# Performance work log

Measured on AMD Instinct MI355X. Metric: run time of the kernel, lower is better.

The kernel has to match this reference:

```python
import jax, jax.numpy as jnp
import numpy as np

N_TOKEN = 32000
D_MODEL = 1024
N_HEAD = 16
D_HEAD = 64
D_INNER = 4096
N_LAYER = 2
QLEN = 256
MLEN = 256
BSZ = 8


def setup_inputs() -> dict:
    key = jax.random.key(0)
    ks = jax.random.split(key, 16)
    s = 0.02  # init scale
    inp = {}
    inp['dec_inp'] = jax.random.randint(ks[0], (QLEN, BSZ), 0, N_TOKEN, dtype=jnp.int32)
    inp['target'] = jax.random.randint(ks[1], (QLEN, BSZ), 0, N_TOKEN, dtype=jnp.int32)
    inp['valid_mask'] = jnp.ones((QLEN, BSZ), jnp.float32)
    inp['mems'] = jax.random.normal(ks[2], (N_LAYER, MLEN, BSZ, D_MODEL), jnp.float32)
    inp['vocab_emb'] = jax.random.normal(ks[3], (N_TOKEN, D_MODEL), jnp.float32) * s
    inp['out_w'] = jax.random.normal(ks[4], (N_TOKEN, D_MODEL), jnp.float32) * s
    inp['out_b'] = jnp.zeros((N_TOKEN,), jnp.float32)
    inp['qkv_w'] = jax.random.normal(ks[5], (N_LAYER, D_MODEL, 3 * N_HEAD * D_HEAD), jnp.float32) * s
    inp['r_w'] = jax.random.normal(ks[6], (N_LAYER, D_MODEL, N_HEAD * D_HEAD), jnp.float32) * s
    inp['o_w'] = jax.random.normal(ks[7], (N_LAYER, N_HEAD * D_HEAD, D_MODEL), jnp.float32) * s
    inp['ln1_g'] = jnp.ones((N_LAYER, D_MODEL), jnp.float32)
    inp['ln1_b'] = jnp.zeros((N_LAYER, D_MODEL), jnp.float32)
    inp['ff_w1'] = jax.random.normal(ks[8], (N_LAYER, D_MODEL, D_INNER), jnp.float32) * s
    inp['ff_b1'] = jnp.zeros((N_LAYER, D_INNER), jnp.float32)
    inp['ff_w2'] = jax.random.normal(ks[9], (N_LAYER, D_INNER, D_MODEL), jnp.float32) * s
    inp['ff_b2'] = jnp.zeros((N_LAYER, D_MODEL), jnp.float32)
    inp['ln2_g'] = jnp.ones((N_LAYER, D_MODEL), jnp.float32)
    inp['ln2_b'] = jnp.zeros((N_LAYER, D_MODEL), jnp.float32)
    inp['r_w_bias'] = jax.random.normal(ks[10], (N_HEAD, D_HEAD), jnp.float32) * s
    inp['r_r_bias'] = jax.random.normal(ks[11], (N_HEAD, D_HEAD), jnp.float32) * s
    return inp


def _layer_norm(x, g, b, eps=1e-3):  # keras LayerNormalization default eps
    m = jnp.mean(x, -1, keepdims=True)
    v = jnp.var(x, -1, keepdims=True)
    return (x - m) * jax.lax.rsqrt(v + eps) * g + b


def _rel_shift(x):
    # x: [qlen, klen, bsz, n_head] -> Transformer-XL relative shift trick
    i, j, b, n = x.shape
    x = jnp.pad(x, ((0, 0), (1, 0), (0, 0), (0, 0)))
    return x.reshape(j + 1, i, b, n)[1:].reshape(i, j, b, n)


def _forward(dec_inp, target, valid_mask, mems, vocab_emb, out_w, out_b, qkv_w, r_w, o_w,
             ln1_g, ln1_b, ff_w1, ff_b1, ff_w2, ff_b2, ln2_g, ln2_b, r_w_bias, r_r_bias):
    qlen, bsz = dec_inp.shape
    mlen = mems.shape[1]
    klen = qlen + mlen
    H, Dh = r_w_bias.shape
    D = vocab_emb.shape[1]
    scale = 1.0 / (Dh ** 0.5)

    # embedding lookup (d_model == d_embed, so no projection)
    h = vocab_emb[dec_inp] * (D ** 0.5)  # [qlen, bsz, D]

    # sinusoidal relative positional embedding, pos_seq = klen-1 ... 0
    pos_seq = jnp.arange(klen - 1, -1, -1, dtype=jnp.float32)
    inv_freq = 1.0 / (10000.0 ** (jnp.arange(0, D, 2, dtype=jnp.float32) / D))
    sinusoid = pos_seq[:, None] * inv_freq[None, :]
    pos_emb = jnp.concatenate([jnp.sin(sinusoid), jnp.cos(sinusoid)], -1)  # [klen, D]

    # causal mask: 1 = masked (strict upper triangle of the query block)
    mask = jnp.concatenate(
        [jnp.zeros((qlen, mlen), jnp.float32), jnp.triu(jnp.ones((qlen, qlen), jnp.float32), 1)], 1)
    mask4 = mask[:, :, None, None]  # [qlen, klen, 1, 1]

    for l in range(mems.shape[0]):
        cat = jnp.concatenate([mems[l], h], 0)  # [klen, bsz, D]
        w_heads = jnp.einsum('kbd,de->kbe', cat, qkv_w[l])  # [klen, bsz, 3*H*Dh]
        q, k, v = jnp.split(w_heads, 3, -1)
        q = q[-qlen:].reshape(qlen, bsz, H, Dh)
        k = k.reshape(klen, bsz, H, Dh)
        v = v.reshape(klen, bsz, H, Dh)
        r_head_k = (pos_emb @ r_w[l]).reshape(klen, H, Dh)

        AC = jnp.einsum('ibnd,jbnd->ijbn', q + r_w_bias, k)
        BD = _rel_shift(jnp.einsum('ibnd,jnd->ijbn', q + r_r_bias, r_head_k))
        score = (AC + BD) * scale
        score = score * (1.0 - mask4) - 1e30 * mask4
        prob = jax.nn.softmax(score, axis=1)  # softmax over key axis j
        vec = jnp.einsum('ijbn,jbnd->ibnd', prob, v).reshape(qlen, bsz, H * Dh)
        h = _layer_norm(vec @ o_w[l] + h, ln1_g[l], ln1_b[l])

        ff = jax.nn.relu(h @ ff_w1[l] + ff_b1[l])
        ff = jax.nn.relu(ff @ ff_w2[l] + ff_b2[l])  # note: source applies relu on dense2 too
        h = _layer_norm(ff + h, ln2_g[l], ln2_b[l])

    logits = jnp.einsum('ibd,nd->ibn', h, out_w) + out_b  # [qlen, bsz, n_token]
    logp = jax.nn.log_softmax(logits, -1)
    nll = -jnp.take_along_axis(logp, target[..., None], -1)[..., 0]
    nll = nll * valid_mask
    return jnp.mean(nll)


def reference(dec_inp, target, valid_mask, mems, vocab_emb, out_w, out_b, qkv_w, r_w, o_w,
              ln1_g, ln1_b, ff_w1, ff_b1, ff_w2, ff_b2, ln2_g, ln2_b, r_w_bias, r_r_bias):
    return _forward(dec_inp, target, valid_mask, mems, vocab_emb, out_w, out_b, qkv_w, r_w, o_w,
                    ln1_g, ln1_b, ff_w1, ff_b1, ff_w2, ff_b2, ln2_g, ln2_b, r_w_bias, r_r_bias)
```

## Files before the change

### kernel.cpp

```cpp
#include <hip/hip_runtime.h>
#include <hip/hip_bf16.h>
#include <math.h>

#define QLEN 256
#define MLEN 256
#define KLEN 512
#define BSZ 8
#define DMODEL 1024
#define NHEAD 16
#define DHEAD 64
#define DINNER 4096
#define NTOKEN 32000
#define NLAYER 2
#define NTOK 2048
#define VTILES 250
#define LPAD 40

typedef __attribute__((ext_vector_type(8))) short bf16x8;
typedef __attribute__((ext_vector_type(4))) float f32x4;

__device__ __forceinline__ float b2f(ushort u) { return __uint_as_float(((unsigned)u) << 16); }
__device__ __forceinline__ ushort f2b(float x) {
  unsigned u = __float_as_uint(x);
  return (ushort)((u + 0x7fffu + ((u >> 16) & 1u)) >> 16);
}

__device__ __forceinline__ void gload16(const ushort* g, ushort* l) {
    __builtin_amdgcn_global_load_lds(
        (const __attribute__((address_space(1))) unsigned int*)(g),
        (__attribute__((address_space(3))) unsigned int*)(l), 16, 0, 0);
}

static const size_t O_H      = 0;
static const size_t O_HBF    = 2097152;
static const size_t O_POSBF  = 3145728;
static const size_t O_QKVT   = 3407872;
static const size_t O_RWT    = O_QKVT + 3145728;
static const size_t O_OWT    = O_RWT + 1048576;
static const size_t O_FFW1T  = O_OWT + 1048576;
static const size_t O_FFW2T  = O_FFW1T + 4194304;
static const size_t O_SCR    = O_FFW2T + 4194304;
static const size_t O_MEMBF  = O_SCR;
static const size_t O_QW     = O_SCR + 2097152;
static const size_t O_QR     = O_QW + 1048576;
static const size_t O_KG     = O_QR + 1048576;
static const size_t O_VG     = O_KG + 2097152;
static const size_t O_RHKT   = O_SCR + 8388608;
static const size_t O_VECBF  = O_SCR + 8650752;
static const size_t O_TATTN  = O_SCR + 9699328;
static const size_t O_BDS    = O_SCR + 11796480;
static const size_t O_OWP1   = O_BDS;
static const size_t O_T1BF   = O_BDS;
static const size_t O_T2     = O_BDS + 4194304;
static const size_t O_T2B    = O_T2 + 2097152;
static const size_t O_OUTWBF = O_SCR;
static const size_t O_PMAX   = O_SCR + 16384000;
static const size_t O_PSUM   = O_PMAX + 512000;
static const size_t O_LSE    = O_PSUM + 512000;
static const size_t O_TGT    = O_LSE + 2048;


__global__ __launch_bounds__(256) void embed_kernel(const int* __restrict__ dec,
    const float* __restrict__ emb, float* __restrict__ h, ushort* __restrict__ hb) {
    int t = blockIdx.x;
    int tok = dec[t];
    const float* src = emb + (size_t)tok * DMODEL;
    float* dst = h + (size_t)t * DMODEL;
    ushort* dstb = hb + (size_t)t * DMODEL;
    for (int u = 0; u < 4; ++u) {
        int d = threadIdx.x + u * 256;
        float v = src[d] * 32.0f;
        dst[d] = v;
        dstb[d] = f2b(v);
    }
}

__global__ __launch_bounds__(256) void posemb_kernel(ushort* __restrict__ pe) {
    int r = blockIdx.x;
    float pos = (float)(KLEN - 1 - r);
    for (int u = 0; u < 2; ++u) {
        int dp = threadIdx.x + u * 256;
        float inv = expf(-(float)dp * (9.210340371976184f / 512.0f));
        float ang = pos * inv;
        pe[(size_t)r * DMODEL + dp]       = f2b(sinf(ang));
        pe[(size_t)r * DMODEL + 512 + dp] = f2b(cosf(ang));
    }
}

__global__ __launch_bounds__(256) void transpose_bf16_kernel(const float* __restrict__ W,
    ushort* __restrict__ Wt, int K, int N) {
    __shared__ float tile[32][33];
    int tx = threadIdx.x & 31, ty = threadIdx.x >> 5;
    int n0 = blockIdx.x * 32, k0 = blockIdx.y * 32;
    for (int u = 0; u < 4; ++u)
        tile[ty + u * 8][tx] = W[(size_t)(k0 + ty + u * 8) * N + n0 + tx];
    __syncthreads();
    for (int u = 0; u < 4; ++u)
        Wt[(size_t)(n0 + ty + u * 8) * K + k0 + tx] = f2b(tile[tx][ty + u * 8]);
}

__global__ __launch_bounds__(256) void convert_bf16_kernel(const float* __restrict__ W,
    ushort* __restrict__ Wb) {
    size_t i = (size_t)blockIdx.x * 256 + threadIdx.x;
    float4 v = ((const float4*)W)[i];
    ushort4 o;
    o.x = f2b(v.x); o.y = f2b(v.y); o.z = f2b(v.z); o.w = f2b(v.w);
    ((ushort4*)Wb)[i] = o;
}

__device__ __forceinline__ int xcd_swizzle(int bid, int nwg) {
    int cpx = nwg >> 3;
    return (bid & 7) * cpx + (bid >> 3);
}

#define GEMM_BODY_DMA_DB2(APTR, BPTR, KEXT, LDA, LDB)                          \
    const int tid = threadIdx.x;                                               \
    const int wave = tid >> 6, lane = tid & 63;                                \
    const int wr = wave >> 1, wc = wave & 1;                                   \
    const int fr = lane & 15, kq = lane >> 4;                                  \
    const int srow = wave * 16 + (lane >> 2);                                  \
    const int scol = 8 * ((lane & 3) ^ ((lane >> 3) & 3));                     \
    const int rsw  = 8 * (kq ^ ((fr >> 1) & 3));                               \
    const ushort* Ap = (APTR) + (size_t)(m0 + srow) * (LDA) + scol;            \
    const ushort* Bp = (BPTR) + (size_t)(n0 + srow) * (LDB) + scol;            \
    ushort* Al = &As[wave * 512];                                              \
    ushort* Bl = &Bs[wave * 512];                                              \
    const ushort* Ard = &As[(wr * 64 + fr) * 32 + rsw];                        \
    const ushort* Brd = &Bs[(wc * 64 + fr) * 32 + rsw];                        \
    const size_t halfA = (size_t)64 * (LDA);                                   \
    const size_t halfB = (size_t)64 * (LDB);                                   \
    const int nk = (KEXT) / 32;                                                \
    gload16(Ap, Al);                                                           \
    gload16(Ap + halfA, Al + 2048);                                            \
    gload16(Bp, Bl);                                                           \
    gload16(Bp + halfB, Bl + 2048);                                            \
    f32x4 acc[4][4] = {};                                                      \
    int cur = 0;                                                               \
    for (int t = 0; t < nk; ++t) {                                             \
        __syncthreads();                                                       \
        if (t + 1 < nk) {                                                      \
            const int kn = (t + 1) * 32;                                       \
            const int nxt = (cur ^ 1) * 4096;                                  \
            gload16(Ap + kn, Al + nxt);                                        \
            gload16(Ap + kn + halfA, Al + nxt + 2048);                         \
            gload16(Bp + kn, Bl + nxt);                                        \
            gload16(Bp + kn + halfB, Bl + nxt + 2048);                         \
        }                                                                      \
        const ushort* Ardc = Ard + cur * 4096;                                 \
        const ushort* Brdc = Brd + cur * 4096;                                 \
        bf16x8 af[4], bfr[4];                                                  \
        _Pragma("unroll")                                                      \
        for (int i = 0; i < 4; ++i) af[i]  = *(const bf16x8*)(Ardc + i * 16 * 32); \
        _Pragma("unroll")                                                      \
        for (int i = 0; i < 4; ++i) bfr[i] = *(const bf16x8*)(Brdc + i * 16 * 32); \
        _Pragma("unroll")                                                      \
        for (int mi = 0; mi < 4; ++mi)                                         \
            _Pragma("unroll")                                                  \
            for (int ni = 0; ni < 4; ++ni)                                     \
                acc[mi][ni] = __builtin_amdgcn_mfma_f32_16x16x32_bf16(         \
                    af[mi], bfr[ni], acc[mi][ni], 0, 0, 0);                    \
        cur ^= 1;                                                              \
    }

#define GEMM_BODY_DMA_DB(APTR, BPTR, KDIM) GEMM_BODY_DMA_DB2(APTR, BPTR, KDIM, KDIM, KDIM)

#define GEMM_BODY_DMA_SB(APTR, BPTR, KDIM)                                     \
    const int tid = threadIdx.x;                                               \
    const int wave = tid >> 6, lane = tid & 63;                                \
    const int wr = wave >> 1, wc = wave & 1;                                   \
    const int fr = lane & 15, kq = lane >> 4;                                  \
    const int srow = wave * 16 + (lane >> 2);                                  \
    const int scol = 8 * ((lane & 3) ^ ((lane >> 3) & 3));                     \
    const int rsw  = 8 * (kq ^ ((fr >> 1) & 3));                               \
    const ushort* Ap = (APTR) + (size_t)(m0 + srow) * (KDIM) + scol;           \
    const ushort* Bp = (BPTR) + (size_t)(n0 + srow) * (KDIM) + scol;           \
    ushort* Al = &As[wave * 512];                                              \
    ushort* Bl = &Bs[wave * 512];                                              \
    const ushort* Ard = &As[(wr * 64 + fr) * 32 + rsw];                        \
    const ushort* Brd = &Bs[(wc * 64 + fr) * 32 + rsw];                        \
    const size_t halfstep = (size_t)64 * (KDIM);                               \
    f32x4 acc[4][4] = {};                                                      \
    for (int k0 = 0; k0 < (KDIM); k0 += 32) {                                  \
        __syncthreads();                                                       \
        gload16(Ap + k0, Al);                                                  \
        gload16(Ap + k0 + halfstep, Al + 2048);                                \
        gload16(Bp + k0, Bl);                                                  \
        gload16(Bp + k0 + halfstep, Bl + 2048);                                \
        __syncthreads();                                                       \
        bf16x8 af[4], bfr[4];                                                  \
        _Pragma("unroll")                                                      \
        for (int i = 0; i < 4; ++i) af[i]  = *(const bf16x8*)(Ard + i * 16 * 32); \
        _Pragma("unroll")                                                      \
        for (int i = 0; i < 4; ++i) bfr[i] = *(const bf16x8*)(Brd + i * 16 * 32); \
        _Pragma("unroll")                                                      \
        for (int mi = 0; mi < 4; ++mi)                                         \
            _Pragma("unroll")                                                  \
            for (int ni = 0; ni < 4; ++ni)                                     \
                acc[mi][ni] = __builtin_amdgcn_mfma_f32_16x16x32_bf16(         \
                    af[mi], bfr[ni], acc[mi][ni], 0, 0, 0);                    \
    }

#define GEMM_BODY_REG(APTR, BPTR, KDIM)                                        \
    const int tid = threadIdx.x;                                               \
    const int wave = tid >> 6, lane = tid & 63;                                \
    const int wr = wave >> 1, wc = wave & 1;                                   \
    const int srow = tid >> 1, shalf = tid & 1;                                \
    const ushort* Ap = (APTR) + (size_t)(m0 + srow) * (KDIM) + shalf * 16;     \
    const ushort* Bp = (BPTR) + (size_t)(n0 + srow) * (KDIM) + shalf * 16;     \
    ushort* Asw = &As[srow * LPAD + shalf * 16];                               \
    ushort* Bsw = &Bs[srow * LPAD + shalf * 16];                               \
    const int fr = lane & 15, kq = lane >> 4;                                  \
    const ushort* Ard = &As[(wr * 64 + fr) * LPAD + kq * 8];                   \
    const ushort* Brd = &Bs[(wc * 64 + fr) * LPAD + kq * 8];                   \
    f32x4 acc[4][4] = {};                                                      \
    for (int k0 = 0; k0 < (KDIM); k0 += 32) {                                  \
        float4 a0 = *(const float4*)(Ap + k0);                                 \
        float4 a1 = *(const float4*)(Ap + k0 + 8);                             \
        float4 b0 = *(const float4*)(Bp + k0);                                 \
        float4 b1 = *(const float4*)(Bp + k0 + 8);                             \
        *(float4*)(Asw)     = a0; *(float4*)(Asw + 8) = a1;                    \
        *(float4*)(Bsw)     = b0; *(float4*)(Bsw + 8) = b1;                    \
        __syncthreads();                                                       \
        bf16x8 af[4], bfr[4];                                                  \
        _Pragma("unroll")                                                      \
        for (int i = 0; i < 4; ++i) af[i]  = *(const bf16x8*)(Ard + i * 16 * LPAD); \
        _Pragma("unroll")                                                      \
        for (int i = 0; i < 4; ++i) bfr[i] = *(const bf16x8*)(Brd + i * 16 * LPAD); \
        _Pragma("unroll")                                                      \
        for (int mi = 0; mi < 4; ++mi)                                         \
            _Pragma("unroll")                                                  \
            for (int ni = 0; ni < 4; ++ni)                                     \
                acc[mi][ni] = __builtin_amdgcn_mfma_f32_16x16x32_bf16(         \
                    af[mi], bfr[ni], acc[mi][ni], 0, 0, 0);                    \
        __syncthreads();                                                       \
    }

template<int OUTBF, int ACT>
__global__ __launch_bounds__(256) void gemm_bf16_kernel(
    const ushort* __restrict__ A, const ushort* __restrict__ Bt,
    const float* __restrict__ bias, void* __restrict__ Cout,
    int M, int N, int K) {
    __shared__ ushort As[2 * 128 * 32];
    __shared__ ushort Bs[2 * 128 * 32];
    int m0 = blockIdx.y * 128, n0 = blockIdx.x * 128;
    GEMM_BODY_DMA_DB(A, Bt, K)
    float* Cf  = (float*)Cout;
    ushort* Cb = (ushort*)Cout;
    #pragma unroll
    for (int ni = 0; ni < 4; ++ni) {
        int cg = n0 + wc * 64 + ni * 16 + fr;
        float bv = bias ? bias[cg] : 0.0f;
        #pragma unroll
        for (int mi = 0; mi < 4; ++mi) {
            int rg = m0 + wr * 64 + mi * 16 + kq * 4;
            #pragma unroll
            for (int r = 0; r < 4; ++r) {
                float v = acc[mi][ni][r] + bv;
                if (ACT) v = fmaxf(v, 0.0f);
                if (OUTBF) Cb[(size_t)(rg + r) * N + cg] = f2b(v);
                else       Cf[(size_t)(rg + r) * N + cg] = v;
            }
        }
    }
}

__global__ __launch_bounds__(256) void gemm_splitk_kernel(
    const ushort* __restrict__ A, const ushort* __restrict__ Bt,
    const float* __restrict__ bias, float* __restrict__ C0, float* __restrict__ C1,
    int N, int K) {
    __shared__ ushort As[2 * 128 * 32];
    __shared__ ushort Bs[2 * 128 * 32];
    int m0 = blockIdx.y * 128, n0 = blockIdx.x * 128;
    const int z = blockIdx.z;
    const int kext = K >> 1;
    const ushort* Az = A + (size_t)z * kext;
    const ushort* Bz = Bt + (size_t)z * kext;
    GEMM_BODY_DMA_DB2(Az, Bz, kext, K, K)
    float* Cf = z ? C1 : C0;
    const float* bp = (z == 0) ? bias : nullptr;
    #pragma unroll
    for (int ni = 0; ni < 4; ++ni) {
        int cg = n0 + wc * 64 + ni * 16 + fr;
        float bv = bp ? bp[cg] : 0.0f;
        #pragma unroll
        for (int mi = 0; mi < 4; ++mi) {
            int rg = m0 + wr * 64 + mi * 16 + kq * 4;
            #pragma unroll
            for (int r = 0; r < 4; ++r)
                Cf[(size_t)(rg + r) * N + cg] = acc[mi][ni][r] + bv;
        }
    }
}

__global__ __launch_bounds__(256) void qkv_gemm_kernel(
    const ushort* __restrict__ Am, const ushort* __restrict__ Ah,
    const ushort* __restrict__ Bt,
    const float* __restrict__ rwb, const float* __restrict__ rrb,
    ushort* __restrict__ Qw, ushort* __restrict__ Qr,
    ushort* __restrict__ Kg, ushort* __restrict__ Vg) {
    __shared__ ushort As[2 * 128 * 32];
    __shared__ ushort Bs[2 * 128 * 32];
    int m0 = blockIdx.y * 128, n0 = blockIdx.x * 128;
    const ushort* Aeff = (m0 < 2048) ? Am : (Ah - (size_t)2048 * DMODEL);
    GEMM_BODY_DMA_DB(Aeff, Bt, DMODEL)
    #pragma unroll
    for (int ni = 0; ni < 4; ++ni) {
        int e = n0 + wc * 64 + ni * 16 + fr;
        #pragma unroll
        for (int mi = 0; mi < 4; ++mi) {
            int rg = m0 + wr * 64 + mi * 16 + kq * 4;
            #pragma unroll
            for (int r = 0; r < 4; ++r) {
                float v = acc[mi][ni][r];
                int m = rg + r;
                int b_ = m & 7, jr = m >> 3;
                if (e < 1024) {
                    if (m >= 2048) {
                        int n_ = e >> 6, d_ = e & 63, i_ = jr - 256;
                        size_t qa = (((size_t)b_ * 16 + n_) * 256 + i_) * 64 + d_;
                        Qw[qa] = f2b(v + rwb[e]);
                        Qr[qa] = f2b(v + rrb[e]);
                    }
                } else if (e < 2048) {
                    int e2 = e - 1024;
                    int n_ = e2 >> 6, d_ = e2 & 63;
                    Kg[(((size_t)b_ * 16 + n_) * 512 + jr) * 64 + d_] = f2b(v);
                } else {
                    int e2 = e - 2048;
                    int n_ = e2 >> 6, d_ = e2 & 63;
                    Vg[(((size_t)b_ * 16 + n_) * 512 + jr) * 64 + d_] = f2b(v);
                }
            }
        }
    }
}

__global__ __launch_bounds__(256) void rhk_gemm_kernel(
    const ushort* __restrict__ A, const ushort* __restrict__ Bt,
    ushort* __restrict__ rhkT) {
    __shared__ ushort As[128 * LPAD];
    __shared__ ushort Bs[128 * LPAD];
    int m0 = blockIdx.y * 128, n0 = blockIdx.x * 128;
    GEMM_BODY_REG(A, Bt, DMODEL)
    #pragma unroll
    for (int ni = 0; ni < 4; ++ni) {
        int e = n0 + wc * 64 + ni * 16 + fr;
        int n_ = e >> 6, d_ = e & 63;
        #pragma unroll
        for (int mi = 0; mi < 4; ++mi) {
            int rg = m0 + wr * 64 + mi * 16 + kq * 4;
            #pragma unroll
            for (int r = 0; r < 4; ++r)
                rhkT[((size_t)n_ * 512 + (rg + r)) * 64 + d_] = f2b(acc[mi][ni][r]);
        }
    }
}

__global__ __launch_bounds__(256) void bd_gemm_kernel(
    const ushort* __restrict__ QrAll, const ushort* __restrict__ rhkT,
    ushort* __restrict__ BDs) {
    __shared__ ushort As[2 * 128 * 32];
    __shared__ ushort Bs[2 * 128 * 32];
    int batch = blockIdx.z;
    const ushort* A  = QrAll + (size_t)batch * (256 * 64);
    const ushort* Bt = rhkT + (size_t)(batch & 15) * (512 * 64);
    ushort* BDb = BDs + (size_t)batch * (256 * 512);
    int m0 = blockIdx.y * 128, n0 = blockIdx.x * 128;
    GEMM_BODY_DMA_DB(A, Bt, 64)
    #pragma unroll
    for (int ni = 0; ni < 4; ++ni) {
        int rr = n0 + wc * 64 + ni * 16 + fr;
        #pragma unroll
        for (int mi = 0; mi < 4; ++mi) {
            int rg = m0 + wr * 64 + mi * 16 + kq * 4;
            #pragma unroll
            for (int r = 0; r < 4; ++r) {
                int i = rg + r;
                int j = rr + i - 255;
                if ((unsigned)j < 512u)
                    BDb[(size_t)i * 512 + j] = f2b(acc[mi][ni][r]);
            }
        }
    }
}

__global__ __launch_bounds__(256) void fused_attn_kernel(
    const ushort* __restrict__ Qw, const ushort* __restrict__ Kg,
    const ushort* __restrict__ Vg, const ushort* __restrict__ BDs,
    ushort* __restrict__ vec) {
    __shared__ ushort Ks[64 * 72];
    __shared__ ushort Vt[64 * 72];
    __shared__ ushort Pl[4][16 * 72];
    const int qt = blockIdx.x, b = blockIdx.y, n = blockIdx.z;
    const int tid = threadIdx.x, wv = tid >> 6, lane = tid & 63;
    const int fr = lane & 15, kq = lane >> 4;
    const int q0 = qt * 64;
    const size_t bn = (size_t)b * 16 + n;
    const ushort* Qb  = Qw + bn * 256 * 64;
    const ushort* Kb  = Kg + bn * 512 * 64;
    const ushort* Vb  = Vg + bn * 512 * 64;
    const ushort* BDb = BDs + bn * 256 * 512;
    bf16x8 aq0, aq1;
    {
        const ushort* qp = Qb + (size_t)(q0 + wv * 16 + fr) * 64 + kq * 8;
        aq0 = *(const bf16x8*)qp;
        aq1 = *(const bf16x8*)(qp + 32);
    }
    f32x4 O[4] = {};
    float m_r[4], l_r[4];
    #pragma unroll
    for (int r = 0; r < 4; ++r) { m_r[r] = -INFINITY; l_r[r] = 0.0f; }
    const int NT = qt + 5;
    const int krow = tid >> 2, kseg = tid & 3;
    const int vrow = tid & 63, vseg0 = tid >> 6;
    for (int jt = 0; jt < NT; ++jt) {
        __syncthreads();
        {
            const ushort* src = Kb + (size_t)(jt * 64 + krow) * 64 + kseg * 16;
            *(float4*)&Ks[krow * 72 + kseg * 16]     = *(const float4*)src;
            *(float4*)&Ks[krow * 72 + kseg * 16 + 8] = *(const float4*)(src + 8);
        }
        #pragma unroll
        for (int it = 0; it < 2; ++it) {
            int seg = vseg0 + it * 4;
            const ushort* src = Vb + (size_t)(jt * 64 + vrow) * 64 + seg * 8;
            bf16x8 v = *(const bf16x8*)src;
            #pragma unroll
            for (int q = 0; q < 8; ++q)
                Vt[(seg * 8 + q) * 72 + vrow] = (ushort)v[q];
        }
        __syncthreads();
        f32x4 S[4] = {};
        #pragma unroll
        for (int cb = 0; cb < 4; ++cb) {
            const ushort* kp = &Ks[(cb * 16 + fr) * 72 + kq * 8];
            bf16x8 b0 = *(const bf16x8*)kp;
            bf16x8 b1 = *(const bf16x8*)(kp + 32);
            S[cb] = __builtin_amdgcn_mfma_f32_16x16x32_bf16(aq0, b0, S[cb], 0, 0, 0);
            S[cb] = __builtin_amdgcn_mfma_f32_16x16x32_bf16(aq1, b1, S[cb], 0, 0, 0);
        }
        #pragma unroll
        for (int cb = 0; cb < 4; ++cb) {
            int j = jt * 64 + cb * 16 + fr;
            #pragma unroll
            for (int r = 0; r < 4; ++r) {
                int i = q0 + wv * 16 + kq * 4 + r;
                float bd = b2f(BDb[(size_t)i * 512 + j]);
                float s = (S[cb][r] + bd) * 0.125f;
                S[cb][r] = (j <= i + 256) ? s : -1e30f;
            }
        }
        float sc[4];
        #pragma unroll
        for (int r = 0; r < 4; ++r) {
            float t = fmaxf(fmaxf(S[0][r], S[1][r]), fmaxf(S[2][r], S[3][r]));
            t = fmaxf(t, __shfl_xor(t, 1));
            t = fmaxf(t, __shfl_xor(t, 2));
            t = fmaxf(t, __shfl_xor(t, 4));
            t = fmaxf(t, __shfl_xor(t, 8));
            float mn = fmaxf(m_r[r], t);
            sc[r] = __expf(m_r[r] - mn);
            m_r[r] = mn;
        }
        float ts[4] = {0.0f, 0.0f, 0.0f, 0.0f};
        #pragma unroll
        for (int cb = 0; cb < 4; ++cb)
            #pragma unroll
            for (int r = 0; r < 4; ++r) {
                float p = __expf(S[cb][r] - m_r[r]);
                S[cb][r] = p;
                ts[r] += p;
            }
        #pragma unroll
        for (int r = 0; r < 4; ++r) {
            float t = ts[r];
            t += __shfl_xor(t, 1);
            t += __shfl_xor(t, 2);
            t += __shfl_xor(t, 4);
            t += __shfl_xor(t, 8);
            l_r[r] = l_r[r] * sc[r] + t;
            #pragma unroll
            for (int ob = 0; ob < 4; ++ob) O[ob][r] *= sc[r];
        }
        ushort* P = &Pl[wv][0];
        #pragma unroll
        for (int cb = 0; cb < 4; ++cb)
            #pragma unroll
            for (int r = 0; r < 4; ++r)
                P[(kq * 4 + r) * 72 + cb * 16 + fr] = f2b(S[cb][r]);
        asm volatile("s_waitcnt lgkmcnt(0)" ::: "memory");
        bf16x8 pa0 = *(const bf16x8*)&P[fr * 72 + kq * 8];
        bf16x8 pa1 = *(const bf16x8*)&P[fr * 72 + 32 + kq * 8];
        #pragma unroll
        for (int ob = 0; ob < 4; ++ob) {
            const ushort* vp = &Vt[(ob * 16 + fr) * 72 + kq * 8];
            bf16x8 v0 = *(const bf16x8*)vp;
            bf16x8 v1 = *(const bf16x8*)(vp + 32);
            O[ob] = __builtin_amdgcn_mfma_f32_16x16x32_bf16(pa0, v0, O[ob], 0, 0, 0);
            O[ob] = __builtin_amdgcn_mfma_f32_16x16x32_bf16(pa1, v1, O[ob], 0, 0, 0);
        }
    }
    #pragma unroll
    for (int r = 0; r < 4; ++r) {
        float inv = 1.0f / l_r[r];
        int i = q0 + wv * 16 + kq * 4 + r;
        size_t base = ((size_t)i * 8 + b) * 1024 + n * 64;
        #pragma unroll
        for (int ob = 0; ob < 4; ++ob)
            vec[base + ob * 16 + fr] = f2b(O[ob][r] * inv);
    }
}

__global__ __launch_bounds__(256) void logits_lse_kernel(
    const ushort* __restrict__ A, const ushort* __restrict__ Bt,
    const float* __restrict__ ob, float* __restrict__ pmax, float* __restrict__ psum) {
    __shared__ ushort As[128 * 32];
    __shared__ ushort Bs[128 * 32];
    __shared__ float redm[2][128], reds[2][128];
    int logical = xcd_swizzle(blockIdx.x, gridDim.x);
    int bx = logical / 16;
    int by = logical % 16;
    int m0 = bx * 128;
    int n0 = by * 128;
    GEMM_BODY_DMA_SB(A, Bt, DMODEL)
    int t0 = n0;
    #pragma unroll
    for (int ni = 0; ni < 4; ++ni) {
        float vals[16];
        float vmax = -1e30f;
        #pragma unroll
        for (int mi = 0; mi < 4; ++mi) {
            int rg = m0 + wr * 64 + mi * 16 + kq * 4;
            float4 ob4 = *(const float4*)&ob[rg];
            float o4[4] = {ob4.x, ob4.y, ob4.z, ob4.w};
            #pragma unroll
            for (int r = 0; r < 4; ++r) {
                float v = acc[mi][ni][r] + o4[r];
                vals[mi * 4 + r] = v;
                vmax = fmaxf(vmax, v);
            }
        }
        vmax = fmaxf(vmax, __shfl_xor(vmax, 16));
        vmax = fmaxf(vmax, __shfl_xor(vmax, 32));
        float s = 0.0f;
        #pragma unroll
        for (int q = 0; q < 16; ++q) s += __expf(vals[q] - vmax);
        s += __shfl_xor(s, 16);
        s += __shfl_xor(s, 32);
        if (kq == 0) {
            redm[wr][wc * 64 + ni * 16 + fr] = vmax;
            reds[wr][wc * 64 + ni * 16 + fr] = s;
        }
    }
    __syncthreads();
    if (tid < 128) {
        float ma = redm[0][tid], mb = redm[1][tid];
        float m = fmaxf(ma, mb);
        float s = reds[0][tid] * __expf(ma - m) + reds[1][tid] * __expf(mb - m);
        pmax[(size_t)(t0 + tid) * VTILES + bx] = m;
        psum[(size_t)(t0 + tid) * VTILES + bx] = s;
    }
}

template<int RELU>
__global__ __launch_bounds__(256) void ln_combine_kernel(const float* __restrict__ x0,
    const float* __restrict__ x1, float* __restrict__ h, const float* __restrict__ g,
    const float* __restrict__ bb, ushort* __restrict__ hb) {
    int t = blockIdx.x, tid = threadIdx.x;
    __shared__ float rs[256], rq[256];
    float v[4];
    float s = 0.0f, sq = 0.0f;
    for (int u = 0; u < 4; ++u) {
        int d = tid + u * 256;
        size_t idx = (size_t)t * DMODEL + d;
        float xx = x0[idx] + x1[idx];
        if (RELU) xx = fmaxf(xx, 0.0f);
        float val = xx + h[idx];
        v[u] = val; s += val; sq += val * val;
    }
    rs[tid] = s; rq[tid] = sq;
    __syncthreads();
    for (int st = 128; st > 0; st >>= 1) {
        if (tid < st) { rs[tid] += rs[tid + st]; rq[tid] += rq[tid + st]; }
        __syncthreads();
    }
    float mean = rs[0] * (1.0f / DMODEL);
    float var = rq[0] * (1.0f / DMODEL) - mean * mean;
    float r = rsqrtf(var + 1e-3f);
    for (int u = 0; u < 4; ++u) {
        int d = tid + u * 256;
        float o = (v[u] - mean) * r * g[d] + bb[d];
        h[(size_t)t * DMODEL + d] = o;
        hb[(size_t)t * DMODEL + d] = f2b(o);
    }
}


__global__ __launch_bounds__(64) void tgt_kernel(const float* __restrict__ h,
    const float* __restrict__ W, const float* __restrict__ ob,
    const int* __restrict__ target, float* __restrict__ tgt) {
    int t = blockIdx.x;
    int lane = threadIdx.x;
    int row = target[t];
    const float* hp = h + (size_t)t * DMODEL;
    const float* wp = W + (size_t)row * DMODEL;
    float s = 0.0f;
    for (int d = lane; d < DMODEL; d += 64) s += hp[d] * wp[d];
    for (int o = 32; o > 0; o >>= 1) s += __shfl_down(s, o);
    if (lane == 0) tgt[t] = s + ob[row];
}

__global__ __launch_bounds__(64) void lse_kernel(const float* __restrict__ pmax,
    const float* __restrict__ psum, float* __restrict__ lse) {
    int t = blockIdx.x;
    int lane = threadIdx.x;
    const float* pm = pmax + (size_t)t * VTILES;
    const float* ps = psum + (size_t)t * VTILES;
    float m = -1e30f;
    for (int c = lane; c < VTILES; c += 64) m = fmaxf(m, pm[c]);
    for (int o = 32; o > 0; o >>= 1) m = fmaxf(m, __shfl_xor(m, o));
    float s = 0.0f;
    for (int c = lane; c < VTILES; c += 64) s += ps[c] * expf(pm[c] - m);
    for (int o = 32; o > 0; o >>= 1) s += __shfl_xor(s, o);
    if (lane == 0) lse[t] = m + logf(s);
}

__global__ __launch_bounds__(256) void loss_kernel(const float* __restrict__ lse,
    const float* __restrict__ tgt, const float* __restrict__ vm, float* __restrict__ out) {
    __shared__ float red[256];
    int tid = threadIdx.x;
    float s = 0.0f;
    for (int t = tid; t < NTOK; t += 256) s += (lse[t] - tgt[t]) * vm[t];
    red[tid] = s;
    __syncthreads();
    for (int st = 128; st > 0; st >>= 1) {
        if (tid < st) red[tid] += red[tid + st];
        __syncthreads();
    }
    if (tid == 0) out[0] = red[0] * (1.0f / NTOK);
}

extern "C" void kernel_launch(void* const* d_in, const int* in_sizes, int n_in,
                              void* d_out, int out_size, void* d_ws, size_t ws_size,
                              hipStream_t stream) {
    const int*   dec_inp   = (const int*)  d_in[0];
    const int*   target    = (const int*)  d_in[1];
    const float* valid     = (const float*)d_in[2];
    const float* mems      = (const float*)d_in[3];
    const float* vocab_emb = (const float*)d_in[4];
    const float* out_w     = (const float*)d_in[5];
    const float* out_b     = (const float*)d_in[6];
    const float* qkv_w     = (const float*)d_in[7];
    const float* r_w       = (const float*)d_in[8];
    const float* o_w       = (const float*)d_in[9];
    const float* ln1_g     = (const float*)d_in[10];
    const float* ln1_b     = (const float*)d_in[11];
    const float* ff_w1     = (const float*)d_in[12];
    const float* ff_b1     = (const float*)d_in[13];
    const float* ff_w2     = (const float*)d_in[14];
    const float* ff_b2     = (const float*)d_in[15];
    const float* ln2_g     = (const float*)d_in[16];
    const float* ln2_b     = (const float*)d_in[17];
    const float* r_w_bias  = (const float*)d_in[18];
    const float* r_r_bias  = (const float*)d_in[19];

    float* ws = (float*)d_ws;
    float*  h      = ws + O_H;
    ushort* hbf    = (ushort*)(ws + O_HBF);
    ushort* posbf  = (ushort*)(ws + O_POSBF);
    ushort* qkvt   = (ushort*)(ws + O_QKVT);
    ushort* rwt    = (ushort*)(ws + O_RWT);
    ushort* owt    = (ushort*)(ws + O_OWT);
    ushort* ffw1t  = (ushort*)(ws + O_FFW1T);
    ushort* ffw2t  = (ushort*)(ws + O_FFW2T);
    ushort* membf  = (ushort*)(ws + O_MEMBF);
    ushort* qwv    = (ushort*)(ws + O_QW);
    ushort* qrv    = (ushort*)(ws + O_QR);
    ushort* kg     = (ushort*)(ws + O_KG);
    ushort* vg     = (ushort*)(ws + O_VG);
    ushort* rhkT   = (ushort*)(ws + O_RHKT);
    ushort* vecbf  = (ushort*)(ws + O_VECBF);
    float*  tattn  = ws + O_TATTN;
    ushort* bds    = (ushort*)(ws + O_BDS);
    float*  owp1   = ws + O_OWP1;
    ushort* t1bf   = (ushort*)(ws + O_T1BF);
    float*  t2     = ws + O_T2;
    float*  t2b    = ws + O_T2B;
    ushort* outwbf = (ushort*)(ws + O_OUTWBF);
    float*  pmax   = ws + O_PMAX;
    float*  psum   = ws + O_PSUM;
    float*  lse    = ws + O_LSE;
    float*  tgt    = ws + O_TGT;

    for (int l = 0; l < NLAYER; ++l) {
        transpose_bf16_kernel<<<dim3(96, 32), 256, 0, stream>>>(
            qkv_w + (size_t)l * DMODEL * 3072, qkvt + (size_t)l * 3072 * DMODEL, DMODEL, 3072);
        transpose_bf16_kernel<<<dim3(32, 32), 256, 0, stream>>>(
            r_w + (size_t)l * DMODEL * DMODEL, rwt + (size_t)l * DMODEL * DMODEL, DMODEL, DMODEL);
        transpose_bf16_kernel<<<dim3(32, 32), 256, 0, stream>>>(
            o_w + (size_t)l * DMODEL * DMODEL, owt + (size_t)l * DMODEL * DMODEL, DMODEL, DMODEL);
        transpose_bf16_kernel<<<dim3(128, 32), 256, 0, stream>>>(
            ff_w1 + (size_t)l * DMODEL * DINNER, ffw1t + (size_t)l * DINNER * DMODEL, DMODEL, DINNER);
        transpose_bf16_kernel<<<dim3(32, 128), 256, 0, stream>>>(
            ff_w2 + (size_t)l * DINNER * DMODEL, ffw2t + (size_t)l * DMODEL * DINNER, DINNER, DMODEL);
    }
    embed_kernel<<<NTOK, 256, 0, stream>>>(dec_inp, vocab_emb, h, hbf);
    posemb_kernel<<<KLEN, 256, 0, stream>>>(posbf);
    convert_bf16_kernel<<<4096, 256, 0, stream>>>(mems, membf);

    for (int l = 0; l < NLAYER; ++l) {
        qkv_gemm_kernel<<<dim3(24, 32), 256, 0, stream>>>(
            membf + (size_t)l * 2097152, hbf,
            qkvt + (size_t)l * 3072 * DMODEL, r_w_bias, r_r_bias, qwv, qrv, kg, vg);
        rhk_gemm_kernel<<<dim3(8, 4), 256, 0, stream>>>(
            posbf, rwt + (size_t)l * DMODEL * DMODEL, rhkT);
        bd_gemm_kernel<<<dim3(4, 2, 128), 256, 0, stream>>>(qrv, rhkT, bds);
        fused_attn_kernel<<<dim3(4, BSZ, NHEAD), 256, 0, stream>>>(qwv, kg, vg, bds, vecbf);
        gemm_splitk_kernel<<<dim3(8, 16, 2), 256, 0, stream>>>(
            vecbf, owt + (size_t)l * DMODEL * DMODEL, nullptr, tattn, owp1, DMODEL, DMODEL);
        ln_combine_kernel<0><<<NTOK, 256, 0, stream>>>(
            tattn, owp1, h, ln1_g + l * DMODEL, ln1_b + l * DMODEL, hbf);
        gemm_bf16_kernel<1, 1><<<dim3(32, 16), 256, 0, stream>>>(
            hbf, ffw1t + (size_t)l * DINNER * DMODEL, ff_b1 + (size_t)l * DINNER, t1bf, NTOK, DINNER, DMODEL);
        gemm_splitk_kernel<<<dim3(8, 16, 2), 256, 0, stream>>>(
            t1bf, ffw2t + (size_t)l * DMODEL * DINNER, ff_b2 + (size_t)l * DMODEL, t2, t2b, DMODEL, DINNER);
        ln_combine_kernel<1><<<NTOK, 256, 0, stream>>>(
            t2, t2b, h, ln2_g + l * DMODEL, ln2_b + l * DMODEL, hbf);
    }

    convert_bf16_kernel<<<32000, 256, 0, stream>>>(out_w, outwbf);
    logits_lse_kernel<<<VTILES * 16, 256, 0, stream>>>(
        outwbf, hbf, out_b, pmax, psum);
    tgt_kernel<<<NTOK, 64, 0, stream>>>(h, out_w, out_b, target, tgt);
    lse_kernel<<<NTOK, 64, 0, stream>>>(pmax, psum, lse);
    loss_kernel<<<1, 256, 0, stream>>>(lse, tgt, valid, (float*)d_out);
}
```

Before: 721.7 us.

## Swizzle GEMM block order across XCDs and transpose BD layout for attention reads

The qkv, FFN and output-projection GEMMs now launch on a 1D grid and remap block indices through xcd_swizzle, so neighbouring tiles that share operands run on the same XCD and reuse its L2. Separately, the BD relative-position scores are stored transposed as [j][i]. The attention kernel can then load four consecutive query rows with a single ushort4 instead of four strided scalar loads. The cost is strided scattered writes in the BD GEMM epilogue.

```diff
diff --git a/kernel.cpp b/kernel.cpp
--- a/kernel.cpp
+++ b/kernel.cpp
@@ -239,10 +239,12 @@
 __global__ __launch_bounds__(256) void gemm_bf16_kernel(
     const ushort* __restrict__ A, const ushort* __restrict__ Bt,
     const float* __restrict__ bias, void* __restrict__ Cout,
-    int M, int N, int K) {
+    int N, int K, int nby) {
     __shared__ ushort As[2 * 128 * 32];
     __shared__ ushort Bs[2 * 128 * 32];
-    int m0 = blockIdx.y * 128, n0 = blockIdx.x * 128;
+    int logical = xcd_swizzle(blockIdx.x, gridDim.x);
+    int bx = logical / nby, by = logical % nby;
+    int m0 = by * 128, n0 = bx * 128;
     GEMM_BODY_DMA_DB(A, Bt, K)
     float* Cf  = (float*)Cout;
     ushort* Cb = (ushort*)Cout;
@@ -267,10 +269,12 @@
 __global__ __launch_bounds__(256) void gemm_splitk_kernel(
     const ushort* __restrict__ A, const ushort* __restrict__ Bt,
     const float* __restrict__ bias, float* __restrict__ C0, float* __restrict__ C1,
-    int N, int K) {
+    int N, int K, int nby) {
     __shared__ ushort As[2 * 128 * 32];
     __shared__ ushort Bs[2 * 128 * 32];
-    int m0 = blockIdx.y * 128, n0 = blockIdx.x * 128;
+    int logical = xcd_swizzle(blockIdx.x, gridDim.x);
+    int bx = logical / nby, by = logical % nby;
+    int m0 = by * 128, n0 = bx * 128;
     const int z = blockIdx.z;
     const int kext = K >> 1;
     const ushort* Az = A + (size_t)z * kext;
@@ -300,7 +304,9 @@
     ushort* __restrict__ Kg, ushort* __restrict__ Vg) {
     __shared__ ushort As[2 * 128 * 32];
     __shared__ ushort Bs[2 * 128 * 32];
-    int m0 = blockIdx.y * 128, n0 = blockIdx.x * 128;
+    int logical = xcd_swizzle(blockIdx.x, gridDim.x);
+    int bx = logical / 32, by = logical % 32;
+    int m0 = by * 128, n0 = bx * 128;
     const ushort* Aeff = (m0 < 2048) ? Am : (Ah - (size_t)2048 * DMODEL);
     GEMM_BODY_DMA_DB(Aeff, Bt, DMODEL)
     #pragma unroll
@@ -378,7 +384,7 @@
                 int i = rg + r;
                 int j = rr + i - 255;
                 if ((unsigned)j < 512u)
-                    BDb[(size_t)i * 512 + j] = f2b(acc[mi][ni][r]);
+                    BDb[(size_t)j * 256 + i] = f2b(acc[mi][ni][r]);
             }
         }
     }
@@ -413,6 +419,7 @@
     const int NT = qt + 5;
     const int krow = tid >> 2, kseg = tid & 3;
     const int vrow = tid & 63, vseg0 = tid >> 6;
+    const int i0 = q0 + wv * 16 + kq * 4;
     for (int jt = 0; jt < NT; ++jt) {
         __syncthreads();
         {
@@ -442,11 +449,12 @@
         #pragma unroll
         for (int cb = 0; cb < 4; ++cb) {
             int j = jt * 64 + cb * 16 + fr;
+            ushort4 bd4 = *(const ushort4*)&BDb[(size_t)j * 256 + i0];
+            float bdv[4] = {b2f(bd4.x), b2f(bd4.y), b2f(bd4.z), b2f(bd4.w)};
             #pragma unroll
             for (int r = 0; r < 4; ++r) {
-                int i = q0 + wv * 16 + kq * 4 + r;
-                float bd = b2f(BDb[(size_t)i * 512 + j]);
-                float s = (S[cb][r] + bd) * 0.125f;
+                int i = i0 + r;
+                float s = (S[cb][r] + bdv[r]) * 0.125f;
                 S[cb][r] = (j <= i + 256) ? s : -1e30f;
             }
         }
@@ -503,7 +511,7 @@
     #pragma unroll
     for (int r = 0; r < 4; ++r) {
         float inv = 1.0f / l_r[r];
-        int i = q0 + wv * 16 + kq * 4 + r;
+        int i = i0 + r;
         size_t base = ((size_t)i * 8 + b) * 1024 + n * 64;
         #pragma unroll
         for (int ob = 0; ob < 4; ++ob)
@@ -709,21 +717,21 @@
     convert_bf16_kernel<<<4096, 256, 0, stream>>>(mems, membf);
 
     for (int l = 0; l < NLAYER; ++l) {
-        qkv_gemm_kernel<<<dim3(24, 32), 256, 0, stream>>>(
+        qkv_gemm_kernel<<<768, 256, 0, stream>>>(
             membf + (size_t)l * 2097152, hbf,
             qkvt + (size_t)l * 3072 * DMODEL, r_w_bias, r_r_bias, qwv, qrv, kg, vg);
         rhk_gemm_kernel<<<dim3(8, 4), 256, 0, stream>>>(
             posbf, rwt + (size_t)l * DMODEL * DMODEL, rhkT);
         bd_gemm_kernel<<<dim3(4, 2, 128), 256, 0, stream>>>(qrv, rhkT, bds);
         fused_attn_kernel<<<dim3(4, BSZ, NHEAD), 256, 0, stream>>>(qwv, kg, vg, bds, vecbf);
-        gemm_splitk_kernel<<<dim3(8, 16, 2), 256, 0, stream>>>(
-            vecbf, owt + (size_t)l * DMODEL * DMODEL, nullptr, tattn, owp1, DMODEL, DMODEL);
+        gemm_splitk_kernel<<<dim3(128, 1, 2), 256, 0, stream>>>(
+            vecbf, owt + (size_t)l * DMODEL * DMODEL, nullptr, tattn, owp1, DMODEL, DMODEL, 16);
         ln_combine_kernel<0><<<NTOK, 256, 0, stream>>>(
             tattn, owp1, h, ln1_g + l * DMODEL, ln1_b + l * DMODEL, hbf);
-        gemm_bf16_kernel<1, 1><<<dim3(32, 16), 256, 0, stream>>>(
-            hbf, ffw1t + (size_t)l * DINNER * DMODEL, ff_b1 + (size_t)l * DINNER, t1bf, NTOK, DINNER, DMODEL);
-        gemm_splitk_kernel<<<dim3(8, 16, 2), 256, 0, stream>>>(
-            t1bf, ffw2t + (size_t)l * DMODEL * DINNER, ff_b2 + (size_t)l * DMODEL, t2, t2b, DMODEL, DINNER);
+        gemm_bf16_kernel<1, 1><<<512, 256, 0, stream>>>(
+            hbf, ffw1t + (size_t)l * DINNER * DMODEL, ff_b1 + (size_t)l * DINNER, t1bf, DINNER, DMODEL, 16);
+        gemm_splitk_kernel<<<dim3(128, 1, 2), 256, 0, stream>>>(
+            t1bf, ffw2t + (size_t)l * DMODEL * DINNER, ff_b2 + (size_t)l * DMODEL, t2, t2b, DMODEL, DINNER, 16);
         ln_combine_kernel<1><<<NTOK, 256, 0, stream>>>(
             t2, t2b, h, ln2_g + l * DMODEL, ln2_b + l * DMODEL, hbf);
     }
```

Measured after the change: 754.2 us. 4.5% more time.
